# Optimization experiments

Measured on AMD Instinct MI355X. Metric: run time of the kernel, lower is better.

## Reference

```python
import jax, jax.numpy as jnp
import numpy as np

MAX_DEG = 6
N_ATOMS = 500000
BATCH = 1024
F_IN = 75
# atoms are sorted by degree (DeepChem ConvMol convention); counts for degree 0..6
DEG_COUNTS = [20000, 80000, 150000, 150000, 75000, 20000, 5000]
OFF = np.cumsum([0] + DEG_COUNTS)


def setup_inputs():
    key = jax.random.key(0)
    ks = jax.random.split(key, 20)

    def p(k, shape):
        return jax.random.normal(k, shape, jnp.float32) * 0.05

    inp = {}
    inp["atom_features"] = jax.random.normal(ks[0], (N_ATOMS, F_IN), jnp.float32)
    inp["membership"] = jax.random.randint(ks[1], (N_ATOMS,), 0, BATCH)
    for d in range(1, MAX_DEG + 1):
        inp[f"adj{d}"] = jax.random.randint(ks[1 + d], (DEG_COUNTS[d], d), 0, N_ATOMS)
    inp["gc1_Wn"] = p(ks[8], (MAX_DEG, F_IN, 64))
    inp["gc1_Ws"] = p(ks[9], (MAX_DEG + 1, F_IN, 64))
    inp["gc1_b"] = jnp.zeros((MAX_DEG + 1, 64), jnp.float32)
    inp["gc2_Wn"] = p(ks[10], (MAX_DEG, 64, 64))
    inp["gc2_Ws"] = p(ks[11], (MAX_DEG + 1, 64, 64))
    inp["gc2_b"] = jnp.zeros((MAX_DEG + 1, 64), jnp.float32)
    inp["bn1_gamma"] = jnp.ones((64,), jnp.float32)
    inp["bn1_beta"] = jnp.zeros((64,), jnp.float32)
    inp["bn1_mean"] = jnp.zeros((64,), jnp.float32)
    inp["bn1_var"] = jnp.ones((64,), jnp.float32)
    inp["bn3_gamma"] = jnp.ones((128,), jnp.float32)
    inp["bn3_beta"] = jnp.zeros((128,), jnp.float32)
    inp["bn3_mean"] = jnp.zeros((128,), jnp.float32)
    inp["bn3_var"] = jnp.ones((128,), jnp.float32)
    inp["d1_W"] = p(ks[12], (64, 128))
    inp["d1_b"] = jnp.zeros((128,), jnp.float32)
    inp["d2_W"] = p(ks[13], (256, 64))
    inp["d2_b"] = jnp.zeros((64,), jnp.float32)
    inp["d3_W"] = p(ks[14], (64, 1))
    inp["d3_b"] = jnp.zeros((1,), jnp.float32)
    return inp


def batch_norm(x, gamma, beta, mean, var, eps=1e-3):
    # keras BatchNormalization in inference mode (eps = keras default 1e-3)
    return gamma * (x - mean) * jax.lax.rsqrt(var + eps) + beta


def graph_conv(feat, adjs, Wn, Ws, b):
    # degree-0 atoms: self transform only
    outs = [feat[OFF[0]:OFF[1]] @ Ws[0] + b[0]]
    for d in range(1, MAX_DEG + 1):
        summed = feat[adjs[d - 1]].sum(axis=1)        # [n_d, F] neighbor-sum gather
        self_a = feat[OFF[d]:OFF[d + 1]]              # [n_d, F] atoms of degree d
        outs.append(summed @ Wn[d - 1] + self_a @ Ws[d] + b[d])
    return jnp.tanh(jnp.concatenate(outs, axis=0))


def graph_pool(feat, adjs):
    outs = [feat[OFF[0]:OFF[1]]]                      # degree-0: passthrough
    for d in range(1, MAX_DEG + 1):
        gathered = feat[adjs[d - 1]]                  # [n_d, d, F]
        self_a = feat[OFF[d]:OFF[d + 1]][:, None, :]  # [n_d, 1, F]
        outs.append(jnp.max(jnp.concatenate([self_a, gathered], axis=1), axis=1))
    return jnp.concatenate(outs, axis=0)


def graph_gather(feat, membership):
    s = jax.ops.segment_sum(feat, membership, num_segments=BATCH)
    m = jax.ops.segment_max(feat, membership, num_segments=BATCH)
    return jnp.tanh(jnp.concatenate([s, m], axis=1))  # [BATCH, 2F]


def reference(atom_features, membership, adj1, adj2, adj3, adj4, adj5, adj6,
              gc1_Wn, gc1_Ws, gc1_b, gc2_Wn, gc2_Ws, gc2_b,
              bn1_gamma, bn1_beta, bn1_mean, bn1_var,
              bn3_gamma, bn3_beta, bn3_mean, bn3_var,
              d1_W, d1_b, d2_W, d2_b, d3_W, d3_b):
    adjs = [adj1, adj2, adj3, adj4, adj5, adj6]
    h = graph_conv(atom_features, adjs, gc1_Wn, gc1_Ws, gc1_b)
    h = batch_norm(h, bn1_gamma, bn1_beta, bn1_mean, bn1_var)
    h = graph_pool(h, adjs)
    h = graph_conv(h, adjs, gc2_Wn, gc2_Ws, gc2_b)
    # NOTE: source code reuses self.batch_norm1 after gc2 (batch_norm2 is unused)
    h = batch_norm(h, bn1_gamma, bn1_beta, bn1_mean, bn1_var)
    h = graph_pool(h, adjs)
    h = jnp.tanh(h @ d1_W + d1_b)
    h = batch_norm(h, bn3_gamma, bn3_beta, bn3_mean, bn3_var)
    g = graph_gather(h, membership)                   # [BATCH, 256]
    g = jax.nn.sigmoid(g @ d2_W + d2_b)
    return g @ d3_W + d3_b                            # [BATCH, 1]
```

## Files before the change

kernel.cpp:

```cpp
#include <hip/hip_runtime.h>
#include <hip/hip_fp16.h>
#include <math.h>


struct AdjPtrs { const int* p[6]; };

typedef _Float16 f16x8 __attribute__((ext_vector_type(8)));
typedef float f32x4 __attribute__((ext_vector_type(4)));

#define SORT_NB 512
#define SORT_CHUNK 977

__device__ __forceinline__ float tanh_fast(float x) {
  float ax = fabsf(x);
  float r = __expf(-2.f * ax);
  float t = 1.f - 2.f * r * __builtin_amdgcn_rcpf(1.f + r);
  return copysignf(t, x);
}

__device__ __forceinline__ f16x8 max8(f16x8 a, f16x8 b) {
  #pragma unroll
  for (int i = 0; i < 8; i++) a[i] = (a[i] > b[i]) ? a[i] : b[i];
  return a;
}

__global__ __launch_bounds__(256) void k_hist_blk(const int* __restrict__ mem,
                                                  int* __restrict__ hist2) {
  __shared__ int lh[1024];
  int blk = blockIdx.x, tid = threadIdx.x;
  for (int i = tid; i < 1024; i += 256) lh[i] = 0;
  __syncthreads();
  int base = blk * SORT_CHUNK;
  int end = min(base + SORT_CHUNK, 500000);
  for (int i = base + tid; i < end; i += 256)
    atomicAdd(&lh[mem[i]], 1);
  __syncthreads();
  for (int i = tid; i < 1024; i += 256)
    hist2[blk * 1024 + i] = lh[i];
}

__global__ __launch_bounds__(512) void k_scan_blk(int* __restrict__ hist2,
                                                  int* __restrict__ hist) {
  __shared__ int sc[SORT_NB];
  int key = blockIdx.x, t = threadIdx.x;
  int v = hist2[t * 1024 + key];
  sc[t] = v;
  __syncthreads();
  for (int off = 1; off < SORT_NB; off <<= 1) {
    int u = (t >= off) ? sc[t - off] : 0;
    __syncthreads();
    sc[t] += u;
    __syncthreads();
  }
  hist2[t * 1024 + key] = sc[t] - v;
  if (t == SORT_NB - 1) hist[key] = sc[SORT_NB - 1];
}

__global__ __launch_bounds__(1024) void k_scan(const int* __restrict__ hist,
                                               int* __restrict__ start) {
  __shared__ int sc[1024];
  int t = threadIdx.x;
  int h = hist[t];
  sc[t] = h;
  __syncthreads();
  for (int off = 1; off < 1024; off <<= 1) {
    int v = (t >= off) ? sc[t - off] : 0;
    __syncthreads();
    sc[t] += v;
    __syncthreads();
  }
  start[t] = sc[t] - h;
}

__global__ __launch_bounds__(256) void k_scatter_blk(const int* __restrict__ mem,
                                                     const int* __restrict__ start,
                                                     const int* __restrict__ hist2,
                                                     int* __restrict__ list) {
  __shared__ int lh[1024];
  int blk = blockIdx.x, tid = threadIdx.x;
  for (int i = tid; i < 1024; i += 256) lh[i] = 0;
  __syncthreads();
  int base = blk * SORT_CHUNK;
  int end = min(base + SORT_CHUNK, 500000);
  for (int i = base + tid; i < end; i += 256) {
    int key = mem[i];
    int r = atomicAdd(&lh[key], 1);
    list[start[key] + hist2[blk * 1024 + key] + r] = i;
  }
}

__global__ __launch_bounds__(256) void k_prep(const float* __restrict__ feat,
                                              __half2* __restrict__ featH2) {
  int i = blockIdx.x * 256 + threadIdx.x;
  int a = i / 40;
  int jp = i - a * 40;
  int kk = jp * 2;
  float v0 = (kk < 75) ? feat[(size_t)a * 75 + kk] : 0.f;
  float v1 = (kk + 1 < 75) ? feat[(size_t)a * 75 + kk + 1] : 0.f;
  featH2[i] = __floats2half2_rn(v0, v1);
}

__global__ __launch_bounds__(256) void k_prep_w(
    const float* __restrict__ Ws1, const float* __restrict__ Wn1,
    const float* __restrict__ Ws2, const float* __restrict__ Wn2,
    __half* __restrict__ W1H, __half* __restrict__ W2H) {
  int i = blockIdx.x * 256 + threadIdx.x;
  if (i < 71680) {
    int d = i / 10240, r = i - d * 10240;
    int j = r & 7, lane = (r >> 3) & 63, t = r >> 9;
    int n = (t & 3) * 16 + (lane & 15);
    int k = (t >> 2) * 32 + (lane >> 4) * 8 + j;
    float v = 0.f;
    if (k < 75) v = Ws1[d * 4800 + k * 64 + n];
    else if (k >= 80 && k < 155 && d > 0) v = Wn1[(d - 1) * 4800 + (k - 80) * 64 + n];
    W1H[i] = __float2half(v);
  } else {
    int i2 = i - 71680;
    int d = i2 / 8192, r = i2 - d * 8192;
    int j = r & 7, lane = (r >> 3) & 63, t = r >> 9;
    int n = (t & 3) * 16 + (lane & 15);
    int k = (t >> 2) * 32 + (lane >> 4) * 8 + j;
    float v = 0.f;
    if (k < 64) v = Ws2[d * 4096 + k * 64 + n];
    else if (d > 0) v = Wn2[(d - 1) * 4096 + (k - 64) * 64 + n];
    W2H[i2] = __float2half(v);
  }
}

__global__ __launch_bounds__(256) void k_prep_d1(const float* __restrict__ W,
                                                 __half* __restrict__ D1H) {
  int i = blockIdx.x * 256 + threadIdx.x;
  int n = i >> 6, k = i & 63;
  float v = W[k * 128 + n];
  __half hi = __float2half(v);
  D1H[i] = hi;
  D1H[8192 + i] = __float2half(v - __half2float(hi));
}

template<int FP, int NCH, int D>
__device__ __forceinline__ void gcm_run(
    const __half* __restrict__ featH, const int* __restrict__ adj_g,
    int abase, int na, const f16x8* __restrict__ Wf,
    const float* __restrict__ bias_d,
    const float* __restrict__ bng, const float* __restrict__ bnb,
    const float* __restrict__ bnm, const float* __restrict__ bnv,
    __half* __restrict__ out) {
  int tid = threadIdx.x;
  int lane = tid & 63, w = tid >> 6;
  int ln = lane & 15, q = lane >> 4;
  int m = w * 16 + ln;

  int ar[D > 0 ? D : 1];
  if (D > 0) {
    bool ok = (m < na);
    #pragma unroll
    for (int e = 0; e < D; e++) ar[e] = ok ? adj_g[m * D + e] : 0;
  }

  f32x4 acc[4];
  #pragma unroll
  for (int ns = 0; ns < 4; ns++) {
    float bj = bias_d[ns * 16 + ln];
    acc[ns] = (f32x4){bj, bj, bj, bj};
  }

  #pragma unroll
  for (int c = 0; c < NCH; c++) {
    int ksg = c * 32 + q * 8;
    f16x8 af;
    if (ksg < FP) {
      af = *(const f16x8*)(featH + (size_t)(abase + m) * FP + ksg);
    } else if (D > 0) {
      int kb = ksg - FP;
      f16x8 v = *(const f16x8*)(featH + (size_t)ar[0] * FP + kb);
      #pragma unroll
      for (int e = 1; e < D; e++) {
        f16x8 u = *(const f16x8*)(featH + (size_t)ar[e] * FP + kb);
        v = v + u;
      }
      af = v;
    } else {
      af = (f16x8){};
    }
    #pragma unroll
    for (int ns = 0; ns < 4; ns++) {
      f16x8 bf = Wf[(c * 4 + ns) * 64 + lane];
      acc[ns] = __builtin_amdgcn_mfma_f32_16x16x32_f16(af, bf, acc[ns], 0, 0, 0);
    }
  }

  #pragma unroll
  for (int ns = 0; ns < 4; ns++) {
    int j = ns * 16 + ln;
    float scv = bng[j] * rsqrtf(bnv[j] + 1e-3f);
    float shv = bnb[j] - bnm[j] * scv;
    #pragma unroll
    for (int r = 0; r < 4; r++) {
      int atom = w * 16 + q * 4 + r;
      if (atom < na)
        out[(size_t)(abase + atom) * 64 + j] =
            __float2half(tanh_fast(acc[ns][r]) * scv + shv);
    }
  }
}

template<int FP, int NCH>
__global__ __launch_bounds__(256, 6) void k_gcm(
    const __half* __restrict__ featH, AdjPtrs adjs,
    const __half* __restrict__ WtH, const float* __restrict__ bias,
    const float* __restrict__ bng, const float* __restrict__ bnb,
    const float* __restrict__ bnm, const float* __restrict__ bnv,
    __half* __restrict__ out) {
  int bid = blockIdx.x;
  int d, off, end, bloc;
  if      (bid < 313)  { d = 0; bloc = bid;        off = 0;      end = 20000;  }
  else if (bid < 1563) { d = 1; bloc = bid - 313;  off = 20000;  end = 100000; }
  else if (bid < 3907) { d = 2; bloc = bid - 1563; off = 100000; end = 250000; }
  else if (bid < 6251) { d = 3; bloc = bid - 3907; off = 250000; end = 400000; }
  else if (bid < 7423) { d = 4; bloc = bid - 6251; off = 400000; end = 475000; }
  else if (bid < 7736) { d = 5; bloc = bid - 7423; off = 475000; end = 495000; }
  else                 { d = 6; bloc = bid - 7736; off = 495000; end = 500000; }
  int abase = off + bloc * 64;
  int na = min(64, end - abase);
  const int* adj_g = (d > 0) ? adjs.p[d - 1] + (abase - off) * d : (const int*)0;
  const f16x8* Wf = (const f16x8*)WtH + d * (NCH * 4 * 64);
  const float* bias_d = bias + d * 64;

  switch (d) {
    case 0: gcm_run<FP, NCH, 0>(featH, adj_g, abase, na, Wf, bias_d, bng, bnb, bnm, bnv, out); break;
    case 1: gcm_run<FP, NCH, 1>(featH, adj_g, abase, na, Wf, bias_d, bng, bnb, bnm, bnv, out); break;
    case 2: gcm_run<FP, NCH, 2>(featH, adj_g, abase, na, Wf, bias_d, bng, bnb, bnm, bnv, out); break;
    case 3: gcm_run<FP, NCH, 3>(featH, adj_g, abase, na, Wf, bias_d, bng, bnb, bnm, bnv, out); break;
    case 4: gcm_run<FP, NCH, 4>(featH, adj_g, abase, na, Wf, bias_d, bng, bnb, bnm, bnv, out); break;
    case 5: gcm_run<FP, NCH, 5>(featH, adj_g, abase, na, Wf, bias_d, bng, bnb, bnm, bnv, out); break;
    default: gcm_run<FP, NCH, 6>(featH, adj_g, abase, na, Wf, bias_d, bng, bnb, bnm, bnv, out); break;
  }
}

template<int D>
__device__ __forceinline__ f16x8 pool_h_acc(const f16x8* __restrict__ in8,
                                            const int* __restrict__ ad, int sg, f16x8 v) {
  #pragma unroll
  for (int e = 0; e < D; e++) v = max8(v, in8[ad[e] * 8 + sg]);
  return v;
}

__global__ __launch_bounds__(256) void k_pool_h(const f16x8* __restrict__ in8, AdjPtrs adjs,
                                                f16x8* __restrict__ out8) {
  int t = blockIdx.x * 256 + threadIdx.x;
  int atom = t >> 3, sg = t & 7;
  int d, off;
  if      (atom < 20000)  { d = 0; off = 0;      }
  else if (atom < 100000) { d = 1; off = 20000;  }
  else if (atom < 250000) { d = 2; off = 100000; }
  else if (atom < 400000) { d = 3; off = 250000; }
  else if (atom < 475000) { d = 4; off = 400000; }
  else if (atom < 495000) { d = 5; off = 475000; }
  else                    { d = 6; off = 495000; }
  f16x8 v = in8[atom * 8 + sg];
  if (d > 0) {
    const int* ad = adjs.p[d - 1] + (atom - off) * d;
    switch (d) {
      case 1: v = pool_h_acc<1>(in8, ad, sg, v); break;
      case 2: v = pool_h_acc<2>(in8, ad, sg, v); break;
      case 3: v = pool_h_acc<3>(in8, ad, sg, v); break;
      case 4: v = pool_h_acc<4>(in8, ad, sg, v); break;
      case 5: v = pool_h_acc<5>(in8, ad, sg, v); break;
      default: v = pool_h_acc<6>(in8, ad, sg, v); break;
    }
  }
  out8[atom * 8 + sg] = v;
}

__global__ __launch_bounds__(256, 4) void k_dense1f(
    const __half* __restrict__ hD, const int* __restrict__ list,
    const int* __restrict__ start, const int* __restrict__ hist,
    const __half* __restrict__ D1H, const float* __restrict__ d1b,
    const float* __restrict__ g3, const float* __restrict__ b3,
    const float* __restrict__ m3, const float* __restrict__ v3,
    float* __restrict__ g) {
  int b = blockIdx.x, tid = threadIdx.x;
  int lane = tid & 63, w = tid >> 6;
  int ln = lane & 15, q = lane >> 4;
  int stt = start[b], cnt = hist[b];

  float bj[2], sc[2], sh[2];
  #pragma unroll
  for (int nf = 0; nf < 2; nf++) {
    int col = w * 32 + nf * 16 + ln;
    bj[nf] = d1b[col];
    sc[nf] = g3[col] * rsqrtf(v3[col] + 1e-3f);
    sh[nf] = b3[col] - m3[col] * sc[nf];
  }

  float sum[2] = {0.f, 0.f};
  float mx[2] = {-INFINITY, -INFINITY};

  for (int cb = 0; cb < cnt; cb += 64) {
    int nr = min(64, cnt - cb);
    int ridx[4];
    #pragma unroll
    for (int mf = 0; mf < 4; mf++) {
      int row = mf * 16 + ln;
      ridx[mf] = list[stt + cb + min(row, nr - 1)];
    }

    f32x4 acc[4][2];
    #pragma unroll
    for (int mf = 0; mf < 4; mf++)
      #pragma unroll
      for (int nf = 0; nf < 2; nf++) acc[mf][nf] = (f32x4){bj[nf], bj[nf], bj[nf], bj[nf]};

    #pragma unroll
    for (int hl = 1; hl >= 0; hl--) {
      #pragma unroll
      for (int ks = 0; ks < 2; ks++) {
        f16x8 af[4];
        #pragma unroll
        for (int mf = 0; mf < 4; mf++)
          af[mf] = *(const f16x8*)(hD + (size_t)ridx[mf] * 64 + ks * 32 + q * 8);
        #pragma unroll
        for (int nf = 0; nf < 2; nf++) {
          f16x8 bf = *(const f16x8*)(D1H + hl * 8192 +
                                     (w * 32 + nf * 16 + ln) * 64 + ks * 32 + q * 8);
          #pragma unroll
          for (int mf = 0; mf < 4; mf++)
            acc[mf][nf] = __builtin_amdgcn_mfma_f32_16x16x32_f16(af[mf], bf, acc[mf][nf], 0, 0, 0);
        }
      }
    }

    #pragma unroll
    for (int mf = 0; mf < 4; mf++) {
      #pragma unroll
      for (int nf = 0; nf < 2; nf++) {
        #pragma unroll
        for (int r = 0; r < 4; r++) {
          int row = mf * 16 + q * 4 + r;
          if (row < nr) {
            float v = tanh_fast(acc[mf][nf][r]) * sc[nf] + sh[nf];
            sum[nf] += v;
            mx[nf] = fmaxf(mx[nf], v);
          }
        }
      }
    }
  }

  #pragma unroll
  for (int nf = 0; nf < 2; nf++) {
    sum[nf] += __shfl_xor(sum[nf], 16);
    sum[nf] += __shfl_xor(sum[nf], 32);
    mx[nf] = fmaxf(mx[nf], __shfl_xor(mx[nf], 16));
    mx[nf] = fmaxf(mx[nf], __shfl_xor(mx[nf], 32));
  }
  if (q == 0) {
    #pragma unroll
    for (int nf = 0; nf < 2; nf++) {
      int col = w * 32 + nf * 16 + ln;
      g[b * 256 + col] = tanh_fast(sum[nf]);
      g[b * 256 + 128 + col] = tanh_fast(mx[nf]);
    }
  }
}

__global__ __launch_bounds__(64) void k_dense23(
    const float* __restrict__ g, const float* __restrict__ W2,
    const float* __restrict__ b2, const float* __restrict__ W3,
    const float* __restrict__ b3, float* __restrict__ out) {
  __shared__ float gr[256];
  int b = blockIdx.x, j = threadIdx.x;
  ((float4*)gr)[j] = ((const float4*)(g + b * 256))[j];
  __syncthreads();
  float acc = b2[j];
  #pragma unroll 8
  for (int k = 0; k < 256; k++) acc += gr[k] * W2[k * 64 + j];
  float sg = 1.f / (1.f + expf(-acc));
  float p = sg * W3[j];
  #pragma unroll
  for (int off = 32; off >= 1; off >>= 1) p += __shfl_xor(p, off);
  if (j == 0) out[b] = p + b3[0];
}

extern "C" void kernel_launch(void* const* d_in, const int* in_sizes, int n_in,
                              void* d_out, int out_size, void* d_ws, size_t ws_size,
                              hipStream_t stream) {
  const float* feat = (const float*)d_in[0];
  const int*   mem  = (const int*)d_in[1];
  AdjPtrs adjs;
  for (int i = 0; i < 6; i++) adjs.p[i] = (const int*)d_in[2 + i];
  const float* gc1_Wn = (const float*)d_in[8];
  const float* gc1_Ws = (const float*)d_in[9];
  const float* gc1_b  = (const float*)d_in[10];
  const float* gc2_Wn = (const float*)d_in[11];
  const float* gc2_Ws = (const float*)d_in[12];
  const float* gc2_b  = (const float*)d_in[13];
  const float* bn1g = (const float*)d_in[14];
  const float* bn1b = (const float*)d_in[15];
  const float* bn1m = (const float*)d_in[16];
  const float* bn1v = (const float*)d_in[17];
  const float* bn3g = (const float*)d_in[18];
  const float* bn3b = (const float*)d_in[19];
  const float* bn3m = (const float*)d_in[20];
  const float* bn3v = (const float*)d_in[21];
  const float* d1W = (const float*)d_in[22];
  const float* d1b = (const float*)d_in[23];
  const float* d2W = (const float*)d_in[24];
  const float* d2b = (const float*)d_in[25];
  const float* d3W = (const float*)d_in[26];
  const float* d3b = (const float*)d_in[27];
  float* out = (float*)d_out;

  char* w = (char*)d_ws;
  __half* featH = (__half*)(w);
  __half* hA    = (__half*)(w + 80000000LL);
  __half* hB    = (__half*)(w + 144000000LL);
  __half* hC    = (__half*)(w);
  __half* hD    = (__half*)(w + 80000000LL);
  __half* W1H   = (__half*)(w + 210000000LL);
  __half* W2H   = (__half*)(w + 210200000LL);
  __half* D1H   = (__half*)(w + 210330000LL);
  float*  g     = (float*)(w + 210400000LL);
  int* hist     = (int*)(w + 211600000LL);
  int* start    = (int*)(w + 211604096LL);
  int* list     = (int*)(w + 211612288LL);
  int* hist2    = (int*)(w + 144000000LL);

  k_hist_blk<<<SORT_NB, 256, 0, stream>>>(mem, hist2);
  k_scan_blk<<<1024, SORT_NB, 0, stream>>>(hist2, hist);
  k_scan<<<1, 1024, 0, stream>>>(hist, start);
  k_scatter_blk<<<SORT_NB, 256, 0, stream>>>(mem, start, hist2, list);

  k_prep<<<78125, 256, 0, stream>>>(feat, (__half2*)featH);
  k_prep_w<<<504, 256, 0, stream>>>(gc1_Ws, gc1_Wn, gc2_Ws, gc2_Wn, W1H, W2H);
  k_prep_d1<<<32, 256, 0, stream>>>(d1W, D1H);

  k_gcm<80, 5><<<7815, 256, 0, stream>>>(featH, adjs, W1H, gc1_b,
                                         bn1g, bn1b, bn1m, bn1v, hA);
  k_pool_h<<<15625, 256, 0, stream>>>((const f16x8*)hA, adjs, (f16x8*)hB);
  k_gcm<64, 4><<<7815, 256, 0, stream>>>(hB, adjs, W2H, gc2_b,
                                         bn1g, bn1b, bn1m, bn1v, hC);
  k_pool_h<<<15625, 256, 0, stream>>>((const f16x8*)hC, adjs, (f16x8*)hD);
  k_dense1f<<<1024, 256, 0, stream>>>((const __half*)hD, list, start, hist, D1H, d1b,
                                      bn3g, bn3b, bn3m, bn3v, g);
  k_dense23<<<1024, 64, 0, stream>>>(g, d2W, d2b, d3W, d3b, out);
}
```

Before: 592.0 us.

## Tile graph-conv blocks to 128 atoms, vectorise prep, fuse small kernels

The graph-conv kernel now processes two 16-atom M-subtiles per wave, so 128 atoms per block. Each weight fragment load then feeds two MFMAs, and the block count halves. The feature prep kernel writes 8 halves per thread instead of 2, the d1 weight prep is merged into the main weight prep kernel, and dense2/dense3 are fused into the dense1 kernel through shared memory. These cut launches, the global round trip for g, and weight load traffic, at the cost of higher register pressure (occupancy hint lowered from 6 to 5).

```diff
diff --git a/kernel.cpp b/kernel.cpp
--- a/kernel.cpp
+++ b/kernel.cpp
@@ -90,20 +90,27 @@
 }
 
 __global__ __launch_bounds__(256) void k_prep(const float* __restrict__ feat,
-                                              __half2* __restrict__ featH2) {
+                                              f16x8* __restrict__ out8) {
   int i = blockIdx.x * 256 + threadIdx.x;
-  int a = i / 40;
-  int jp = i - a * 40;
-  int kk = jp * 2;
-  float v0 = (kk < 75) ? feat[(size_t)a * 75 + kk] : 0.f;
-  float v1 = (kk + 1 < 75) ? feat[(size_t)a * 75 + kk + 1] : 0.f;
-  featH2[i] = __floats2half2_rn(v0, v1);
+  if (i >= 5000000) return;
+  int a = i / 10;
+  int jp = i - a * 10;
+  int k0 = jp * 8;
+  const float* src = feat + (size_t)a * 75 + k0;
+  f16x8 v;
+  #pragma unroll
+  for (int e = 0; e < 8; e++) {
+    float f = (k0 + e < 75) ? src[e] : 0.f;
+    v[e] = (_Float16)f;
+  }
+  out8[i] = v;
 }
 
 __global__ __launch_bounds__(256) void k_prep_w(
     const float* __restrict__ Ws1, const float* __restrict__ Wn1,
     const float* __restrict__ Ws2, const float* __restrict__ Wn2,
-    __half* __restrict__ W1H, __half* __restrict__ W2H) {
+    const float* __restrict__ d1W,
+    __half* __restrict__ W1H, __half* __restrict__ W2H, __half* __restrict__ D1H) {
   int i = blockIdx.x * 256 + threadIdx.x;
   if (i < 71680) {
     int d = i / 10240, r = i - d * 10240;
@@ -114,7 +121,7 @@
     if (k < 75) v = Ws1[d * 4800 + k * 64 + n];
     else if (k >= 80 && k < 155 && d > 0) v = Wn1[(d - 1) * 4800 + (k - 80) * 64 + n];
     W1H[i] = __float2half(v);
-  } else {
+  } else if (i < 129024) {
     int i2 = i - 71680;
     int d = i2 / 8192, r = i2 - d * 8192;
     int j = r & 7, lane = (r >> 3) & 63, t = r >> 9;
@@ -124,17 +131,14 @@
     if (k < 64) v = Ws2[d * 4096 + k * 64 + n];
     else if (d > 0) v = Wn2[(d - 1) * 4096 + (k - 64) * 64 + n];
     W2H[i2] = __float2half(v);
-  }
-}
-
-__global__ __launch_bounds__(256) void k_prep_d1(const float* __restrict__ W,
-                                                 __half* __restrict__ D1H) {
-  int i = blockIdx.x * 256 + threadIdx.x;
-  int n = i >> 6, k = i & 63;
-  float v = W[k * 128 + n];
-  __half hi = __float2half(v);
-  D1H[i] = hi;
-  D1H[8192 + i] = __float2half(v - __half2float(hi));
+  } else {
+    int i3 = i - 129024;
+    int n = i3 >> 6, k = i3 & 63;
+    float v = d1W[k * 128 + n];
+    __half hi = __float2half(v);
+    D1H[i3] = hi;
+    D1H[8192 + i3] = __float2half(v - __half2float(hi));
+  }
 }
 
 template<int FP, int NCH, int D>
@@ -148,44 +152,54 @@
   int tid = threadIdx.x;
   int lane = tid & 63, w = tid >> 6;
   int ln = lane & 15, q = lane >> 4;
-  int m = w * 16 + ln;
-
-  int ar[D > 0 ? D : 1];
+
+  int ar[2][D > 0 ? D : 1];
   if (D > 0) {
-    bool ok = (m < na);
-    #pragma unroll
-    for (int e = 0; e < D; e++) ar[e] = ok ? adj_g[m * D + e] : 0;
-  }
-
-  f32x4 acc[4];
+    #pragma unroll
+    for (int ms = 0; ms < 2; ms++) {
+      int m = w * 32 + ms * 16 + ln;
+      bool ok = (m < na);
+      #pragma unroll
+      for (int e = 0; e < D; e++)
+        ar[ms][e] = ok ? adj_g[m * D + e] : 0;
+    }
+  }
+
+  f32x4 acc[2][4];
   #pragma unroll
   for (int ns = 0; ns < 4; ns++) {
     float bj = bias_d[ns * 16 + ln];
-    acc[ns] = (f32x4){bj, bj, bj, bj};
+    acc[0][ns] = (f32x4){bj, bj, bj, bj};
+    acc[1][ns] = acc[0][ns];
   }
 
   #pragma unroll
   for (int c = 0; c < NCH; c++) {
     int ksg = c * 32 + q * 8;
-    f16x8 af;
-    if (ksg < FP) {
-      af = *(const f16x8*)(featH + (size_t)(abase + m) * FP + ksg);
-    } else if (D > 0) {
-      int kb = ksg - FP;
-      f16x8 v = *(const f16x8*)(featH + (size_t)ar[0] * FP + kb);
-      #pragma unroll
-      for (int e = 1; e < D; e++) {
-        f16x8 u = *(const f16x8*)(featH + (size_t)ar[e] * FP + kb);
-        v = v + u;
+    f16x8 af[2];
+    #pragma unroll
+    for (int ms = 0; ms < 2; ms++) {
+      int m = w * 32 + ms * 16 + ln;
+      if (ksg < FP) {
+        af[ms] = *(const f16x8*)(featH + (size_t)(abase + m) * FP + ksg);
+      } else if (D > 0) {
+        int kb = ksg - FP;
+        f16x8 v = *(const f16x8*)(featH + (size_t)ar[ms][0] * FP + kb);
+        #pragma unroll
+        for (int e = 1; e < D; e++) {
+          f16x8 u = *(const f16x8*)(featH + (size_t)ar[ms][e] * FP + kb);
+          v = v + u;
+        }
+        af[ms] = v;
+      } else {
+        af[ms] = (f16x8){};
       }
-      af = v;
-    } else {
-      af = (f16x8){};
     }
     #pragma unroll
     for (int ns = 0; ns < 4; ns++) {
       f16x8 bf = Wf[(c * 4 + ns) * 64 + lane];
-      acc[ns] = __builtin_amdgcn_mfma_f32_16x16x32_f16(af, bf, acc[ns], 0, 0, 0);
+      acc[0][ns] = __builtin_amdgcn_mfma_f32_16x16x32_f16(af[0], bf, acc[0][ns], 0, 0, 0);
+      acc[1][ns] = __builtin_amdgcn_mfma_f32_16x16x32_f16(af[1], bf, acc[1][ns], 0, 0, 0);
     }
   }
 
@@ -195,17 +209,20 @@
     float scv = bng[j] * rsqrtf(bnv[j] + 1e-3f);
     float shv = bnb[j] - bnm[j] * scv;
     #pragma unroll
-    for (int r = 0; r < 4; r++) {
-      int atom = w * 16 + q * 4 + r;
-      if (atom < na)
-        out[(size_t)(abase + atom) * 64 + j] =
-            __float2half(tanh_fast(acc[ns][r]) * scv + shv);
+    for (int ms = 0; ms < 2; ms++) {
+      #pragma unroll
+      for (int r = 0; r < 4; r++) {
+        int atom = w * 32 + ms * 16 + q * 4 + r;
+        if (atom < na)
+          out[(size_t)(abase + atom) * 64 + j] =
+              __float2half(tanh_fast(acc[ms][ns][r]) * scv + shv);
+      }
     }
   }
 }
 
 template<int FP, int NCH>
-__global__ __launch_bounds__(256, 6) void k_gcm(
+__global__ __launch_bounds__(256, 5) void k_gcm(
     const __half* __restrict__ featH, AdjPtrs adjs,
     const __half* __restrict__ WtH, const float* __restrict__ bias,
     const float* __restrict__ bng, const float* __restrict__ bnb,
@@ -213,15 +230,15 @@
     __half* __restrict__ out) {
   int bid = blockIdx.x;
   int d, off, end, bloc;
-  if      (bid < 313)  { d = 0; bloc = bid;        off = 0;      end = 20000;  }
-  else if (bid < 1563) { d = 1; bloc = bid - 313;  off = 20000;  end = 100000; }
-  else if (bid < 3907) { d = 2; bloc = bid - 1563; off = 100000; end = 250000; }
-  else if (bid < 6251) { d = 3; bloc = bid - 3907; off = 250000; end = 400000; }
-  else if (bid < 7423) { d = 4; bloc = bid - 6251; off = 400000; end = 475000; }
-  else if (bid < 7736) { d = 5; bloc = bid - 7423; off = 475000; end = 495000; }
-  else                 { d = 6; bloc = bid - 7736; off = 495000; end = 500000; }
-  int abase = off + bloc * 64;
-  int na = min(64, end - abase);
+  if      (bid < 157)  { d = 0; bloc = bid;        off = 0;      end = 20000;  }
+  else if (bid < 782)  { d = 1; bloc = bid - 157;  off = 20000;  end = 100000; }
+  else if (bid < 1954) { d = 2; bloc = bid - 782;  off = 100000; end = 250000; }
+  else if (bid < 3126) { d = 3; bloc = bid - 1954; off = 250000; end = 400000; }
+  else if (bid < 3712) { d = 4; bloc = bid - 3126; off = 400000; end = 475000; }
+  else if (bid < 3869) { d = 5; bloc = bid - 3712; off = 475000; end = 495000; }
+  else                 { d = 6; bloc = bid - 3869; off = 495000; end = 500000; }
+  int abase = off + bloc * 128;
+  int na = min(128, end - abase);
   const int* adj_g = (d > 0) ? adjs.p[d - 1] + (abase - off) * d : (const int*)0;
   const f16x8* Wf = (const f16x8*)WtH + d * (NCH * 4 * 64);
   const float* bias_d = bias + d * 64;
@@ -278,7 +295,11 @@
     const __half* __restrict__ D1H, const float* __restrict__ d1b,
     const float* __restrict__ g3, const float* __restrict__ b3,
     const float* __restrict__ m3, const float* __restrict__ v3,
-    float* __restrict__ g) {
+    const float* __restrict__ W2, const float* __restrict__ b2,
+    const float* __restrict__ W3, const float* __restrict__ b3d,
+    float* __restrict__ out) {
+  __shared__ float gr[256];
+  __shared__ float part[4][64];
   int b = blockIdx.x, tid = threadIdx.x;
   int lane = tid & 63, w = tid >> 6;
   int ln = lane & 15, q = lane >> 4;
@@ -358,28 +379,26 @@
     #pragma unroll
     for (int nf = 0; nf < 2; nf++) {
       int col = w * 32 + nf * 16 + ln;
-      g[b * 256 + col] = tanh_fast(sum[nf]);
-      g[b * 256 + 128 + col] = tanh_fast(mx[nf]);
-    }
-  }
-}
-
-__global__ __launch_bounds__(64) void k_dense23(
-    const float* __restrict__ g, const float* __restrict__ W2,
-    const float* __restrict__ b2, const float* __restrict__ W3,
-    const float* __restrict__ b3, float* __restrict__ out) {
-  __shared__ float gr[256];
-  int b = blockIdx.x, j = threadIdx.x;
-  ((float4*)gr)[j] = ((const float4*)(g + b * 256))[j];
-  __syncthreads();
-  float acc = b2[j];
+      gr[col] = tanh_fast(sum[nf]);
+      gr[128 + col] = tanh_fast(mx[nf]);
+    }
+  }
+  __syncthreads();
+
+  int j = tid & 63, seg = tid >> 6;
+  float a2 = 0.f;
   #pragma unroll 8
-  for (int k = 0; k < 256; k++) acc += gr[k] * W2[k * 64 + j];
-  float sg = 1.f / (1.f + expf(-acc));
-  float p = sg * W3[j];
-  #pragma unroll
-  for (int off = 32; off >= 1; off >>= 1) p += __shfl_xor(p, off);
-  if (j == 0) out[b] = p + b3[0];
+  for (int k = seg * 64; k < seg * 64 + 64; k++) a2 += gr[k] * W2[k * 64 + j];
+  part[seg][j] = a2;
+  __syncthreads();
+  if (tid < 64) {
+    float a = b2[j] + part[0][j] + part[1][j] + part[2][j] + part[3][j];
+    float sg = 1.f / (1.f + expf(-a));
+    float p = sg * W3[j];
+    #pragma unroll
+    for (int off = 32; off >= 1; off >>= 1) p += __shfl_xor(p, off);
+    if (j == 0) out[b] = p + b3d[0];
+  }
 }
 
 extern "C" void kernel_launch(void* const* d_in, const int* in_sizes, int n_in,
@@ -420,7 +439,6 @@
   __half* W1H   = (__half*)(w + 210000000LL);
   __half* W2H   = (__half*)(w + 210200000LL);
   __half* D1H   = (__half*)(w + 210330000LL);
-  float*  g     = (float*)(w + 210400000LL);
   int* hist     = (int*)(w + 211600000LL);
   int* start    = (int*)(w + 211604096LL);
   int* list     = (int*)(w + 211612288LL);
@@ -431,17 +449,16 @@
   k_scan<<<1, 1024, 0, stream>>>(hist, start);
   k_scatter_blk<<<SORT_NB, 256, 0, stream>>>(mem, start, hist2, list);
 
-  k_prep<<<78125, 256, 0, stream>>>(feat, (__half2*)featH);
-  k_prep_w<<<504, 256, 0, stream>>>(gc1_Ws, gc1_Wn, gc2_Ws, gc2_Wn, W1H, W2H);
-  k_prep_d1<<<32, 256, 0, stream>>>(d1W, D1H);
-
-  k_gcm<80, 5><<<7815, 256, 0, stream>>>(featH, adjs, W1H, gc1_b,
+  k_prep<<<19532, 256, 0, stream>>>(feat, (f16x8*)featH);
+  k_prep_w<<<536, 256, 0, stream>>>(gc1_Ws, gc1_Wn, gc2_Ws, gc2_Wn, d1W, W1H, W2H, D1H);
+
+  k_gcm<80, 5><<<3909, 256, 0, stream>>>(featH, adjs, W1H, gc1_b,
                                          bn1g, bn1b, bn1m, bn1v, hA);
   k_pool_h<<<15625, 256, 0, stream>>>((const f16x8*)hA, adjs, (f16x8*)hB);
-  k_gcm<64, 4><<<7815, 256, 0, stream>>>(hB, adjs, W2H, gc2_b,
+  k_gcm<64, 4><<<3909, 256, 0, stream>>>(hB, adjs, W2H, gc2_b,
                                          bn1g, bn1b, bn1m, bn1v, hC);
   k_pool_h<<<15625, 256, 0, stream>>>((const f16x8*)hC, adjs, (f16x8*)hD);
   k_dense1f<<<1024, 256, 0, stream>>>((const __half*)hD, list, start, hist, D1H, d1b,
-                                      bn3g, bn3b, bn3m, bn3v, g);
-  k_dense23<<<1024, 64, 0, stream>>>(g, d2W, d2b, d3W, d3b, out);
-}
+                                      bn3g, bn3b, bn3m, bn3v,
+                                      d2W, d2b, d3W, d3b, out);
+}
```

Measured after the change: 601.8 us. About the same (+1.7%).
